# Kernel tuning notes

Measured on AMD Instinct MI355X. Metric: run time of the kernel, lower is better.

The kernel has to match this reference:

```python
import jax, jax.numpy as jnp
import numpy as np

T, H, O, L = 8192, 512, 256, 5  # num_frames, hidden(=input), output, num_layers


def setup_inputs() -> dict:
    key = jax.random.key(0)
    ks = jax.random.split(key, 16)
    s = 1.0 / np.sqrt(H)
    def w(k, shape):
        return jax.random.uniform(k, shape, jnp.float32, -s, s)
    d = {"x": jax.random.normal(ks[0], (T, H), jnp.float32)}
    names = ["Wz", "Uz", "Wr", "Ur", "Wh", "Uh"]
    for i, n in enumerate(names):
        d[n] = w(ks[1 + i], (L, H, H))
        d["b" + n] = w(ks[7 + i], (L, H))
    d["fcW"] = w(ks[13], (O, H))
    d["fcb"] = w(ks[14], (O,))
    return d


def _gru_forward(x, Wz, Uz, Wr, Ur, Wh, Uh, bWz, bUz, bWr, bUr, bWh, bUh):
    # x: [T, H]; weights: [L, H, H]; biases: [L, H]
    nl, hs = Wz.shape[0], Wz.shape[1]
    h0 = jnp.zeros((nl, hs), x.dtype)

    def time_step(h, x_t):  # h: [L, H], x_t: [H]
        def layer_step(x_in, p):
            wz, uz, wr, ur, wh, uh, bwz, buz, bwr, bur, bwh, buh, h_prev = p
            z = jax.nn.sigmoid(x_in @ wz.T + bwz + h_prev @ uz.T + buz)
            r = jax.nn.sigmoid(x_in @ wr.T + bwr + h_prev @ ur.T + bur)
            h_tilde = jnp.tanh(x_in @ wh.T + bwh + (r * h_prev) @ uh.T + buh)
            h_new = (1.0 - z) * h_prev + z * h_tilde
            return h_new, h_new  # next layer's input is this layer's hidden

        _, h_new = jax.lax.scan(
            layer_step, x_t,
            (Wz, Uz, Wr, Ur, Wh, Uh, bWz, bUz, bWr, bUr, bWh, bUh, h))
        return h_new, h_new[-1]  # carry new stacked state, emit top-layer h

    h_final, outs = jax.lax.scan(time_step, h0, x)
    return outs, h_final  # outs: [T, H], h_final: [L, H]


def reference(x, Wz, Uz, Wr, Ur, Wh, Uh, bWz, bUz, bWr, bUr, bWh, bUh, fcW, fcb):
    outs, h_final = _gru_forward(x, Wz, Uz, Wr, Ur, Wh, Uh,
                                 bWz, bUz, bWr, bUr, bWh, bUh)
    out = outs @ fcW.T + fcb  # [T, O]
    return out, h_final
```

## Files before the change

kernel.cpp:

```cpp
#include <hip/hip_runtime.h>
#include <math.h>

#define TT 8192
#define HH 512
#define LL 5
#define OO 256
#define GG 48
#define NTHR 256
#define RB 64
#define CAP_TAG 1000000u
#define CAP_PRG 200000u

typedef unsigned long long u64;
typedef unsigned u32;


__device__ __forceinline__ float wred(float v) {
#pragma unroll
  for (int off = 32; off > 0; off >>= 1) v += __shfl_xor(v, off, 64);
  return v;
}

__device__ __forceinline__ float sigm(float v) {
  return 1.0f / (1.0f + expf(-v));
}

__device__ __forceinline__ u64 ldA(const u64* p) {
  return __hip_atomic_load((u64*)p, __ATOMIC_RELAXED, __HIP_MEMORY_SCOPE_AGENT);
}
__device__ __forceinline__ void stA(u64* p, u64 v) {
  __hip_atomic_store(p, v, __ATOMIC_RELAXED, __HIP_MEMORY_SCOPE_AGENT);
}
__device__ __forceinline__ u64 pack(u32 tag, float v) {
  return ((u64)tag << 32) | (u64)__float_as_uint(v);
}

__device__ __forceinline__ void poll2(const u64* p0, const u64* p1, u32 tag,
                                      volatile int* dead, float& v0, float& v1) {
  u64 a = ldA(p0), b = ldA(p1);
  u32 n = 0;
  while ((u32)(a >> 32) != tag || (u32)(b >> 32) != tag) {
    if (*dead) break;
    if (++n > CAP_TAG) { *dead = 1; break; }
    __builtin_amdgcn_s_sleep(2);
    if ((u32)(a >> 32) != tag) a = ldA(p0);
    if ((u32)(b >> 32) != tag) b = ldA(p1);
  }
  v0 = __uint_as_float((u32)a);
  v1 = __uint_as_float((u32)b);
}


__global__ void init_ws(u32* __restrict__ p, int n) {
  int stride = gridDim.x * blockDim.x;
  for (int i = blockIdx.x * blockDim.x + threadIdx.x; i < n; i += stride) p[i] = 0u;
}


__launch_bounds__(NTHR, 1)
__global__ void gru_pipeline(
    const float* __restrict__ x,
    const float* __restrict__ Wz, const float* __restrict__ bWz,
    const float* __restrict__ Uz, const float* __restrict__ bUz,
    const float* __restrict__ Wr, const float* __restrict__ bWr,
    const float* __restrict__ Ur, const float* __restrict__ bUr,
    const float* __restrict__ Wh, const float* __restrict__ bWh,
    const float* __restrict__ Uh, const float* __restrict__ bUh,
    u64* __restrict__ hring,
    u64* __restrict__ rring,
    float* __restrict__ htop,
    u32* __restrict__ prog,
    float* __restrict__ dout)
{
  const int blk = blockIdx.x;
  const int l = blk / GG;
  const int g = blk % GG;
  const bool ltop = (l == LL - 1);
  const int base = HH / GG;
  const int rem = HH % GG;
  const int i0 = g * base + (g < rem ? g : rem);
  const int n_i = base + (g < rem ? 1 : 0);

  const int tid = threadIdx.x;
  const int wave = tid >> 6;
  const int lane = tid & 63;
  const int j0 = lane * 8;
  const int j = tid * 2;

  __shared__ float xs[HH];
  __shared__ float hs[HH];
  __shared__ float rh[HH];
  __shared__ float rtmp[16];
  __shared__ float htmp[16];
  __shared__ int dead_s;
  volatile int* dead = &dead_s;
  if (tid == 0) dead_s = 0;

  float wz[3][8], uz[3][8], wr[3][8], ur[3][8], wh[3][8], uh[3][8];
  float bz[3], br[3], bh[3];
  int rowg[3];
  bool act[3];
#pragma unroll
  for (int k = 0; k < 3; ++k) {
    const int rl = wave + 4 * k;
    act[k] = (rl < n_i);
    const int i = i0 + (act[k] ? rl : 0);
    rowg[k] = i;
    if (act[k]) {
      const size_t ro = ((size_t)l * HH + i) * HH + j0;
      *(float4*)&wz[k][0] = *(const float4*)(Wz + ro);
      *(float4*)&wz[k][4] = *(const float4*)(Wz + ro + 4);
      *(float4*)&uz[k][0] = *(const float4*)(Uz + ro);
      *(float4*)&uz[k][4] = *(const float4*)(Uz + ro + 4);
      *(float4*)&wr[k][0] = *(const float4*)(Wr + ro);
      *(float4*)&wr[k][4] = *(const float4*)(Wr + ro + 4);
      *(float4*)&ur[k][0] = *(const float4*)(Ur + ro);
      *(float4*)&ur[k][4] = *(const float4*)(Ur + ro + 4);
      *(float4*)&wh[k][0] = *(const float4*)(Wh + ro);
      *(float4*)&wh[k][4] = *(const float4*)(Wh + ro + 4);
      *(float4*)&uh[k][0] = *(const float4*)(Uh + ro);
      *(float4*)&uh[k][4] = *(const float4*)(Uh + ro + 4);
      bz[k] = bWz[l * HH + i] + bUz[l * HH + i];
      br[k] = bWr[l * HH + i] + bUr[l * HH + i];
      bh[k] = bWh[l * HH + i] + bUh[l * HH + i];
    } else {
      bz[k] = br[k] = bh[k] = 0.f;
#pragma unroll
      for (int q = 0; q < 8; ++q) {
        wz[k][q] = uz[k][q] = wr[k][q] = ur[k][q] = wh[k][q] = uh[k][q] = 0.f;
      }
    }
  }

  u64* my_h = hring + (size_t)l * RB * HH;
  const u64* up_h = hring + (size_t)(l > 0 ? l - 1 : 0) * RB * HH;
  u64* my_r = rring + (size_t)l * 2 * HH;
  u32* my_prog = prog + l * GG + g;
  u32* dn_prog = prog + (l < LL - 1 ? l + 1 : l) * GG;

  float zreg[3], awreg[3];
  zreg[0] = zreg[1] = zreg[2] = 0.f;
  awreg[0] = awreg[1] = awreg[2] = 0.f;

  __syncthreads();

  for (int t = 0; t < TT; ++t) {
    if (l == 0) {
      const float2 v = *(const float2*)&x[(size_t)t * HH + j];
      xs[j] = v.x; xs[j + 1] = v.y;
    } else {
      const u64* s = up_h + (size_t)(t & (RB - 1)) * HH + j;
      float a, b;
      poll2(s, s + 1, (u32)(t + 1), dead, a, b);
      xs[j] = a; xs[j + 1] = b;
    }
    if (t == 0) {
      hs[j] = 0.f; hs[j + 1] = 0.f;
    } else {
      const u64* s = my_h + (size_t)((t - 1) & (RB - 1)) * HH + j;
      float a, b;
      poll2(s, s + 1, (u32)t, dead, a, b);
      hs[j] = a; hs[j + 1] = b;
    }
    if (wave == 3 && !ltop && t >= RB && lane < GG) {
      const u32 need = (u32)(t - RB + 1);
      u32 n = 0;
      while (__hip_atomic_load(&dn_prog[lane], __ATOMIC_RELAXED,
                               __HIP_MEMORY_SCOPE_AGENT) < need) {
        if (*dead) break;
        if (++n > CAP_PRG) { *dead = 1; break; }
        __builtin_amdgcn_s_sleep(16);
      }
    }
    __syncthreads();

    float xv[8], hv[8];
    *(float4*)&xv[0] = *(const float4*)&xs[j0];
    *(float4*)&xv[4] = *(const float4*)&xs[j0 + 4];
    *(float4*)&hv[0] = *(const float4*)&hs[j0];
    *(float4*)&hv[4] = *(const float4*)&hs[j0 + 4];

    if (t == 0) {
#pragma unroll
      for (int k = 0; k < 3; ++k) {
        if (act[k]) {
          float az = 0.f, aw = 0.f;
#pragma unroll
          for (int q = 0; q < 8; ++q) {
            az = fmaf(wz[k][q], xv[q], az);
            aw = fmaf(wh[k][q], xv[q], aw);
          }
          az = wred(az); aw = wred(aw);
          if (lane == 0) htmp[wave + 4 * k] = sigm(az + bz[k]) * tanhf(aw + bh[k]);
        }
      }
      __syncthreads();
      if (wave == 0 && lane < n_i)
        stA(&my_h[(size_t)0 * HH + i0 + lane], pack(1u, htmp[lane]));
      if (ltop && wave == 1 && lane < n_i)
        htop[(size_t)0 * HH + i0 + lane] = htmp[lane];
      if (tid == 0)
        __hip_atomic_store(my_prog, 1u, __ATOMIC_RELAXED, __HIP_MEMORY_SCOPE_AGENT);
      continue;
    }

#pragma unroll
    for (int k = 0; k < 3; ++k) {
      if (act[k]) {
        float ar = 0.f;
#pragma unroll
        for (int q = 0; q < 8; ++q) {
          ar = fmaf(wr[k][q], xv[q], ar);
          ar = fmaf(ur[k][q], hv[q], ar);
        }
        ar = wred(ar);
        if (lane == 0) rtmp[wave + 4 * k] = sigm(ar + br[k]);
      }
    }
    __syncthreads();
    if (wave == 0 && lane < n_i)
      stA(&my_r[(size_t)(t & 1) * HH + i0 + lane], pack((u32)(t + 1), rtmp[lane]));

#pragma unroll
    for (int k = 0; k < 3; ++k) {
      if (act[k]) {
        float az = 0.f, aw = 0.f;
#pragma unroll
        for (int q = 0; q < 8; ++q) {
          az = fmaf(wz[k][q], xv[q], az);
          az = fmaf(uz[k][q], hv[q], az);
          aw = fmaf(wh[k][q], xv[q], aw);
        }
        az = wred(az); aw = wred(aw);
        if (lane == 0) {
          zreg[k] = sigm(az + bz[k]);
          awreg[k] = aw + bh[k];
        }
      }
    }

    {
      const u64* s = my_r + (size_t)(t & 1) * HH + j;
      float r0, r1;
      poll2(s, s + 1, (u32)(t + 1), dead, r0, r1);
      rh[j] = r0 * hs[j];
      rh[j + 1] = r1 * hs[j + 1];
    }
    __syncthreads();

    float rhv[8];
    *(float4*)&rhv[0] = *(const float4*)&rh[j0];
    *(float4*)&rhv[4] = *(const float4*)&rh[j0 + 4];

#pragma unroll
    for (int k = 0; k < 3; ++k) {
      if (act[k]) {
        float u = 0.f;
#pragma unroll
        for (int q = 0; q < 8; ++q) u = fmaf(uh[k][q], rhv[q], u);
        u = wred(u);
        if (lane == 0) {
          const float z = zreg[k];
          const float hp = hs[rowg[k]];
          const float ht = tanhf(awreg[k] + u);
          htmp[wave + 4 * k] = (1.f - z) * hp + z * ht;
        }
      }
    }
    __syncthreads();

    if (wave == 0 && lane < n_i)
      stA(&my_h[(size_t)(t & (RB - 1)) * HH + i0 + lane], pack((u32)(t + 1), htmp[lane]));
    if (ltop && wave == 1 && lane < n_i)
      htop[(size_t)t * HH + i0 + lane] = htmp[lane];
    if (t == TT - 1 && wave == 2 && lane < n_i)
      dout[(size_t)TT * OO + (size_t)l * HH + i0 + lane] = htmp[lane];
    if (tid == 0)
      __hip_atomic_store(my_prog, (u32)(t + 1), __ATOMIC_RELAXED, __HIP_MEMORY_SCOPE_AGENT);
  }
}


__launch_bounds__(256)
__global__ void fc_gemm(const float* __restrict__ A,
                        const float* __restrict__ W,
                        const float* __restrict__ bias,
                        float* __restrict__ C) {
  __shared__ float As[16][68];
  __shared__ float Ws[16][68];
  const int bm = blockIdx.x;
  const int bn = blockIdx.y;
  const int tid = threadIdx.x;
  const int tx = tid & 15;
  const int ty = tid >> 4;
  const int r = tid >> 2;
  const int kc = (tid & 3) * 4;
  float acc[4][4];
#pragma unroll
  for (int a = 0; a < 4; ++a)
#pragma unroll
    for (int b2 = 0; b2 < 4; ++b2) acc[a][b2] = 0.f;

  for (int k0 = 0; k0 < HH; k0 += 16) {
    const float4 a4 = *(const float4*)&A[(size_t)(bm * 64 + r) * HH + k0 + kc];
    const float4 w4 = *(const float4*)&W[(size_t)(bn * 64 + r) * HH + k0 + kc];
    __syncthreads();
    As[kc + 0][r] = a4.x; As[kc + 1][r] = a4.y; As[kc + 2][r] = a4.z; As[kc + 3][r] = a4.w;
    Ws[kc + 0][r] = w4.x; Ws[kc + 1][r] = w4.y; Ws[kc + 2][r] = w4.z; Ws[kc + 3][r] = w4.w;
    __syncthreads();
#pragma unroll
    for (int kk = 0; kk < 16; ++kk) {
      const float4 av = *(const float4*)&As[kk][ty * 4];
      const float4 wv = *(const float4*)&Ws[kk][tx * 4];
      const float avv[4] = {av.x, av.y, av.z, av.w};
      const float wvv[4] = {wv.x, wv.y, wv.z, wv.w};
#pragma unroll
      for (int a = 0; a < 4; ++a)
#pragma unroll
        for (int b2 = 0; b2 < 4; ++b2)
          acc[a][b2] = fmaf(avv[a], wvv[b2], acc[a][b2]);
    }
  }
#pragma unroll
  for (int a = 0; a < 4; ++a) {
    const int row = bm * 64 + ty * 4 + a;
#pragma unroll
    for (int b2 = 0; b2 < 4; ++b2) {
      const int col = bn * 64 + tx * 4 + b2;
      C[(size_t)row * OO + col] = acc[a][b2] + bias[col];
    }
  }
}


extern "C" void kernel_launch(void* const* d_in, const int* in_sizes, int n_in,
                              void* d_out, int out_size, void* d_ws, size_t ws_size,
                              hipStream_t stream) {
  const float* p[15];
  for (int i = 0; i < 15 && i < n_in; ++i) p[i] = (const float*)d_in[i];

  const float *x, *Wz, *bWz, *Uz, *bUz, *Wr, *bWr, *Ur, *bUr, *Wh, *bWh, *Uh, *bUh, *fcW, *fcb;
  x = p[0];
  if (in_sizes[2] == LL * HH) {
    Wz = p[1]; bWz = p[2]; Uz = p[3]; bUz = p[4];
    Wr = p[5]; bWr = p[6]; Ur = p[7]; bUr = p[8];
    Wh = p[9]; bWh = p[10]; Uh = p[11]; bUh = p[12];
  } else {
    Wz = p[1]; Uz = p[2]; Wr = p[3]; Ur = p[4]; Wh = p[5]; Uh = p[6];
    bWz = p[7]; bUz = p[8]; bWr = p[9]; bUr = p[10]; bWh = p[11]; bUh = p[12];
  }
  fcW = p[13]; fcb = p[14];

  u64* hring = (u64*)d_ws;
  u64* rring = hring + (size_t)LL * RB * HH;
  u32* prog = (u32*)(rring + (size_t)LL * 2 * HH);
  float* htop = (float*)(prog + (size_t)LL * GG);

  const int zero_u32 = (int)(((size_t)LL * RB * HH + (size_t)LL * 2 * HH) * 2 + LL * GG);
  init_ws<<<512, 256, 0, stream>>>((u32*)d_ws, zero_u32);

  gru_pipeline<<<LL * GG, NTHR, 0, stream>>>(
      x, Wz, bWz, Uz, bUz, Wr, bWr, Ur, bUr, Wh, bWh, Uh, bUh,
      hring, rring, htop, prog, (float*)d_out);

  fc_gemm<<<dim3(TT / 64, OO / 64), 256, 0, stream>>>(
      htop, fcW, fcb, (float*)d_out);
}
```

Baseline: 45.11 ms.

## Publish gate results directly from lane 0 and fuse polling loops with hot spin

Removes the shared-memory staging (rtmp/htmp) and the extra __syncthreads that came before the global atomic stores of r and h. Each wave's lane 0 now stores its own row directly. The x and h polls are merged into one loop that spins hot for a bounded number of iterations before sleeping, and the r poll gets the same treatment. The progress counter is published earlier, right after inputs are consumed. Together these shorten the per-timestep critical path of the cross-block pipeline. The cost is more polling traffic and reliance on the correctness of publishing progress early.

Result: slower. 63.27 ms (+40.3%).

```diff
diff --git a/kernel.cpp b/kernel.cpp
--- a/kernel.cpp
+++ b/kernel.cpp
@@ -8,7 +8,8 @@
 #define GG 48
 #define NTHR 256
 #define RB 64
-#define CAP_TAG 1000000u
+#define HOT 96u
+#define CAP_TAG 2000000u
 #define CAP_PRG 200000u
 
 typedef unsigned long long u64;
@@ -33,21 +34,6 @@
 }
 __device__ __forceinline__ u64 pack(u32 tag, float v) {
   return ((u64)tag << 32) | (u64)__float_as_uint(v);
-}
-
-__device__ __forceinline__ void poll2(const u64* p0, const u64* p1, u32 tag,
-                                      volatile int* dead, float& v0, float& v1) {
-  u64 a = ldA(p0), b = ldA(p1);
-  u32 n = 0;
-  while ((u32)(a >> 32) != tag || (u32)(b >> 32) != tag) {
-    if (*dead) break;
-    if (++n > CAP_TAG) { *dead = 1; break; }
-    __builtin_amdgcn_s_sleep(2);
-    if ((u32)(a >> 32) != tag) a = ldA(p0);
-    if ((u32)(b >> 32) != tag) b = ldA(p1);
-  }
-  v0 = __uint_as_float((u32)a);
-  v1 = __uint_as_float((u32)b);
 }
 
 
@@ -90,8 +76,6 @@
   __shared__ float xs[HH];
   __shared__ float hs[HH];
   __shared__ float rh[HH];
-  __shared__ float rtmp[16];
-  __shared__ float htmp[16];
   __shared__ int dead_s;
   volatile int* dead = &dead_s;
   if (tid == 0) dead_s = 0;
@@ -138,29 +122,40 @@
   u32* my_prog = prog + l * GG + g;
   u32* dn_prog = prog + (l < LL - 1 ? l + 1 : l) * GG;
 
-  float zreg[3], awreg[3];
+  float zreg[3], awreg[3], hpown[3];
   zreg[0] = zreg[1] = zreg[2] = 0.f;
   awreg[0] = awreg[1] = awreg[2] = 0.f;
 
   __syncthreads();
 
   for (int t = 0; t < TT; ++t) {
-    if (l == 0) {
-      const float2 v = *(const float2*)&x[(size_t)t * HH + j];
-      xs[j] = v.x; xs[j + 1] = v.y;
-    } else {
-      const u64* s = up_h + (size_t)(t & (RB - 1)) * HH + j;
-      float a, b;
-      poll2(s, s + 1, (u32)(t + 1), dead, a, b);
-      xs[j] = a; xs[j + 1] = b;
-    }
-    if (t == 0) {
-      hs[j] = 0.f; hs[j + 1] = 0.f;
-    } else {
-      const u64* s = my_h + (size_t)((t - 1) & (RB - 1)) * HH + j;
-      float a, b;
-      poll2(s, s + 1, (u32)t, dead, a, b);
-      hs[j] = a; hs[j + 1] = b;
+    {
+      const u64* sx = (l > 0) ? up_h + (size_t)(t & (RB - 1)) * HH + j : (const u64*)0;
+      const u64* sh = (t > 0) ? my_h + (size_t)((t - 1) & (RB - 1)) * HH + j : (const u64*)0;
+      const u32 tagx = (u32)(t + 1), tagh = (u32)t;
+      u64 ax = 0, bx = 0, ah = 0, bh2 = 0;
+      if (sx) { ax = ldA(sx); bx = ldA(sx + 1); }
+      if (sh) { ah = ldA(sh); bh2 = ldA(sh + 1); }
+      u32 n = 0;
+      for (;;) {
+        const bool badx = sx && (((u32)(ax >> 32) != tagx) || ((u32)(bx >> 32) != tagx));
+        const bool badh = sh && (((u32)(ah >> 32) != tagh) || ((u32)(bh2 >> 32) != tagh));
+        if (!badx && !badh) break;
+        if (++n > HOT) {
+          __builtin_amdgcn_s_sleep(4);
+          if (*dead) break;
+          if (n > CAP_TAG) { *dead = 1; break; }
+        }
+        if (badx) { ax = ldA(sx); bx = ldA(sx + 1); }
+        if (badh) { ah = ldA(sh); bh2 = ldA(sh + 1); }
+      }
+      if (sx) { xs[j] = __uint_as_float((u32)ax); xs[j + 1] = __uint_as_float((u32)bx); }
+      else {
+        const float2 v = *(const float2*)&x[(size_t)t * HH + j];
+        xs[j] = v.x; xs[j + 1] = v.y;
+      }
+      if (sh) { hs[j] = __uint_as_float((u32)ah); hs[j + 1] = __uint_as_float((u32)bh2); }
+      else { hs[j] = 0.f; hs[j + 1] = 0.f; }
     }
     if (wave == 3 && !ltop && t >= RB && lane < GG) {
       const u32 need = (u32)(t - RB + 1);
@@ -174,11 +169,18 @@
     }
     __syncthreads();
 
+    if (tid == 0)
+      __hip_atomic_store(my_prog, (u32)(t + 1), __ATOMIC_RELAXED, __HIP_MEMORY_SCOPE_AGENT);
+
     float xv[8], hv[8];
     *(float4*)&xv[0] = *(const float4*)&xs[j0];
     *(float4*)&xv[4] = *(const float4*)&xs[j0 + 4];
     *(float4*)&hv[0] = *(const float4*)&hs[j0];
     *(float4*)&hv[4] = *(const float4*)&hs[j0 + 4];
+#pragma unroll
+    for (int k = 0; k < 3; ++k) hpown[k] = hs[rowg[k]];
+
+    u64* hsl = my_h + (size_t)(t & (RB - 1)) * HH;
 
     if (t == 0) {
 #pragma unroll
@@ -191,19 +193,19 @@
             aw = fmaf(wh[k][q], xv[q], aw);
           }
           az = wred(az); aw = wred(aw);
-          if (lane == 0) htmp[wave + 4 * k] = sigm(az + bz[k]) * tanhf(aw + bh[k]);
+          if (lane == 0) {
+            const float hnew = sigm(az + bz[k]) * tanhf(aw + bh[k]);
+            stA(&hsl[rowg[k]], pack(1u, hnew));
+            if (ltop) htop[(size_t)0 * HH + rowg[k]] = hnew;
+          }
         }
       }
       __syncthreads();
-      if (wave == 0 && lane < n_i)
-        stA(&my_h[(size_t)0 * HH + i0 + lane], pack(1u, htmp[lane]));
-      if (ltop && wave == 1 && lane < n_i)
-        htop[(size_t)0 * HH + i0 + lane] = htmp[lane];
-      if (tid == 0)
-        __hip_atomic_store(my_prog, 1u, __ATOMIC_RELAXED, __HIP_MEMORY_SCOPE_AGENT);
       continue;
     }
 
+    u64* rs = my_r + (size_t)(t & 1) * HH;
+    const u32 tag1 = (u32)(t + 1);
 #pragma unroll
     for (int k = 0; k < 3; ++k) {
       if (act[k]) {
@@ -214,12 +216,9 @@
           ar = fmaf(ur[k][q], hv[q], ar);
         }
         ar = wred(ar);
-        if (lane == 0) rtmp[wave + 4 * k] = sigm(ar + br[k]);
-      }
-    }
-    __syncthreads();
-    if (wave == 0 && lane < n_i)
-      stA(&my_r[(size_t)(t & 1) * HH + i0 + lane], pack((u32)(t + 1), rtmp[lane]));
+        if (lane == 0) stA(&rs[rowg[k]], pack(tag1, sigm(ar + br[k])));
+      }
+    }
 
 #pragma unroll
     for (int k = 0; k < 3; ++k) {
@@ -240,11 +239,20 @@
     }
 
     {
-      const u64* s = my_r + (size_t)(t & 1) * HH + j;
-      float r0, r1;
-      poll2(s, s + 1, (u32)(t + 1), dead, r0, r1);
-      rh[j] = r0 * hs[j];
-      rh[j + 1] = r1 * hs[j + 1];
+      const u64* s = rs + j;
+      u64 a = ldA(s), b = ldA(s + 1);
+      u32 n = 0;
+      while ((u32)(a >> 32) != tag1 || (u32)(b >> 32) != tag1) {
+        if (++n > HOT) {
+          __builtin_amdgcn_s_sleep(4);
+          if (*dead) break;
+          if (n > CAP_TAG) { *dead = 1; break; }
+        }
+        if ((u32)(a >> 32) != tag1) a = ldA(s);
+        if ((u32)(b >> 32) != tag1) b = ldA(s + 1);
+      }
+      rh[j]     = __uint_as_float((u32)a) * hs[j];
+      rh[j + 1] = __uint_as_float((u32)b) * hs[j + 1];
     }
     __syncthreads();
 
@@ -261,22 +269,14 @@
         u = wred(u);
         if (lane == 0) {
           const float z = zreg[k];
-          const float hp = hs[rowg[k]];
           const float ht = tanhf(awreg[k] + u);
-          htmp[wave + 4 * k] = (1.f - z) * hp + z * ht;
-        }
-      }
-    }
-    __syncthreads();
-
-    if (wave == 0 && lane < n_i)
-      stA(&my_h[(size_t)(t & (RB - 1)) * HH + i0 + lane], pack((u32)(t + 1), htmp[lane]));
-    if (ltop && wave == 1 && lane < n_i)
-      htop[(size_t)t * HH + i0 + lane] = htmp[lane];
-    if (t == TT - 1 && wave == 2 && lane < n_i)
-      dout[(size_t)TT * OO + (size_t)l * HH + i0 + lane] = htmp[lane];
-    if (tid == 0)
-      __hip_atomic_store(my_prog, (u32)(t + 1), __ATOMIC_RELAXED, __HIP_MEMORY_SCOPE_AGENT);
+          const float hnew = (1.f - z) * hpown[k] + z * ht;
+          stA(&hsl[rowg[k]], pack(tag1, hnew));
+          if (ltop) htop[(size_t)t * HH + rowg[k]] = hnew;
+          if (t == TT - 1) dout[(size_t)TT * OO + (size_t)l * HH + rowg[k]] = hnew;
+        }
+      }
+    }
   }
 }
 
```
